# Optimization experiments

Measured on AMD Instinct MI355X. Metric: run time of the kernel, lower is better.

The kernel has to match this reference:

```python
import jax, jax.numpy as jnp
import numpy as np

HIDDEN = 2048
INTER = 4096
NUM_EXPERTS = 8
TOP_K = 4
BATCH, SEQ = 2, 2048
TOKENS = BATCH * SEQ


def setup_inputs() -> dict:
    key = jax.random.key(0)
    k_x, k_rw, k_tw, k_te, k_gu, k_dn = jax.random.split(key, 6)
    x = jax.random.normal(k_x, (BATCH, SEQ, HIDDEN), dtype=jnp.float32)
    # full router weights (passed through but unused by this patched forward)
    weights = jax.random.uniform(k_rw, (TOKENS, NUM_EXPERTS), dtype=jnp.float32)
    tw = jax.random.uniform(k_tw, (TOKENS, TOP_K), dtype=jnp.float32)
    top_weights = tw / jnp.sum(tw, axis=-1, keepdims=True)  # softmax-like, renormalize=False downstream
    top_experts = jax.random.randint(k_te, (TOKENS, TOP_K), 0, NUM_EXPERTS, dtype=jnp.int64)
    scale_gu = 1.0 / np.sqrt(HIDDEN)
    scale_dn = 1.0 / np.sqrt(INTER)
    gate_up_weights = jax.random.normal(k_gu, (NUM_EXPERTS, 2 * INTER, HIDDEN), dtype=jnp.float32) * scale_gu
    down_weights = jax.random.normal(k_dn, (NUM_EXPERTS, HIDDEN, INTER), dtype=jnp.float32) * scale_dn
    return {
        'x': x,
        'weights': weights,
        'top_weights': top_weights,
        'top_experts': top_experts,
        'gate_up_weights': gate_up_weights,
        'down_weights': down_weights,
    }


def _fused_moe(xf, gate_up_weights, down_weights, top_weights, top_experts):
    """xf: [T, D]. Dense per-expert loop (scan over experts), masked combine.

    Matches fused_moe(renormalize=False): out[t] = sum_k top_weights[t,k] * expert_{top_experts[t,k]}(x[t])
    expert(x) = (silu(x @ Wg^T) * (x @ Wu^T)) @ Wd^T with [Wg; Wu] = gate_up.
    """
    E = gate_up_weights.shape[0]

    def step(out, inp):
        w_gu, w_d, e = inp
        # per-token combine coefficient for this expert (0 if not routed)
        coef = jnp.sum(jnp.where(top_experts == e, top_weights, 0.0), axis=-1)  # [T]
        h = xf @ w_gu.T                       # [T, 2*INTER]
        gate, up = jnp.split(h, 2, axis=-1)
        act = jax.nn.silu(gate) * up          # [T, INTER]
        o = act @ w_d.T                       # [T, D]
        return out + coef[:, None] * o, None

    out, _ = jax.lax.scan(step, jnp.zeros_like(xf),
                          (gate_up_weights, down_weights, jnp.arange(E, dtype=jnp.int64)))
    return out


def reference(x, weights, top_weights, top_experts, gate_up_weights, down_weights):
    B, S, D = x.shape
    xf = x.reshape(-1, D)  # flatten(0, 1)
    out = _fused_moe(xf, gate_up_weights, down_weights, top_weights, top_experts)
    return out.reshape(B, S, D)  # unflatten(0, (-1, q_len))
```

## Files before the change

### kernel.cpp

```cpp
#include <hip/hip_runtime.h>
#include <stdint.h>

#define T_TOKENS 4096
#define D_HID    2048
#define D_INT    4096
#define N_EXP    8
#define TOPK     4
#define NFLAT    (T_TOKENS*TOPK)
#define BMT      256
#define MAXPAD   (NFLAT + N_EXP*BMT)
#define MT2      (MAXPAD/BMT)

#define OFF_PTOK 0ull
#define OFF_PWT  73728ull
#define OFF_CNT  147456ull
#define OFF_TOFF 147712ull
#define OFF_SEG  155904ull
#define OFF_XB   262144ull
#define OFF_ACT  17039360ull
#define OFF_W    168034304ull

typedef float f32x4  __attribute__((ext_vector_type(4)));
typedef short bf16x8 __attribute__((ext_vector_type(8)));

__device__ __forceinline__ unsigned short f2bf(float f) {
    unsigned int u = __float_as_uint(f);
    u += 0x7fffu + ((u >> 16) & 1u);
    return (unsigned short)(u >> 16);
}

__device__ __forceinline__ void gload_lds16(const void* g, void* l) {
    __builtin_amdgcn_global_load_lds((const __attribute__((address_space(1))) void*)g,
                                     (__attribute__((address_space(3))) void*)l,
                                     16, 0, 0);
}

__device__ __forceinline__ int xcd_logical(int hw, int nwg) {
    int q = nwg >> 3, r = nwg & 7;
    int xc = hw & 7, sl = hw >> 3;
    return (xc < r ? xc * (q + 1) : r * (q + 1) + (xc - r) * q) + sl;
}

__global__ void k_prep(const float* __restrict__ x, unsigned short* __restrict__ xb,
                       float* __restrict__ out) {
    const int N4 = T_TOKENS * D_HID / 4;
    for (int i = blockIdx.x * 256 + threadIdx.x; i < N4; i += 2048 * 256) {
        float4 v = ((const float4*)x)[i];
        ushort4 h;
        h.x = f2bf(v.x); h.y = f2bf(v.y); h.z = f2bf(v.z); h.w = f2bf(v.w);
        ((ushort4*)xb)[i] = h;
        ((float4*)out)[i] = make_float4(0.f, 0.f, 0.f, 0.f);
    }
}

__global__ void k_cast(const float* __restrict__ src, unsigned short* __restrict__ dst, int n4) {
    for (int i = blockIdx.x * 256 + threadIdx.x; i < n4; i += 2048 * 256) {
        float4 v = ((const float4*)src)[i];
        ushort4 h;
        h.x = f2bf(v.x); h.y = f2bf(v.y); h.z = f2bf(v.z); h.w = f2bf(v.w);
        ((ushort4*)dst)[i] = h;
    }
}

__global__ void k_count(const int* __restrict__ te, int* __restrict__ counts,
                        int* __restrict__ toff) {
    int e = blockIdx.x, t = threadIdx.x;
    int cnt = 0;
    int base = t * 64;
    for (int i = 0; i < 64; i++) cnt += (te[base + i] == e);
    __shared__ int s[256];
    s[t] = cnt; __syncthreads();
    int incl = cnt;
    for (int off = 1; off < 256; off <<= 1) {
        int tmp = (t >= off) ? s[t - off] : 0;
        __syncthreads();
        incl += tmp; s[t] = incl;
        __syncthreads();
    }
    toff[e * 256 + t] = incl - cnt;
    if (t == 255) counts[e] = incl;
}

__global__ void k_fill(const int* __restrict__ te, const float* __restrict__ tw,
                       const int* __restrict__ counts, const int* __restrict__ toff,
                       int* __restrict__ ptok, float* __restrict__ pwt, int* __restrict__ seg) {
    int e = blockIdx.x, t = threadIdx.x;
    int segs[9]; int a = 0;
    #pragma unroll
    for (int j = 0; j < 8; j++) { segs[j] = a; a += (counts[j] + BMT - 1) & ~(BMT - 1); }
    segs[8] = a;
    if (e == 0 && t == 0) { for (int j = 0; j < 9; j++) seg[j] = segs[j]; }
    int base = segs[e] + toff[e * 256 + t];
    int rank = 0;
    for (int i = t * 64; i < (t + 1) * 64; i++) {
        if (te[i] == e) { ptok[base + rank] = i >> 2; pwt[base + rank] = tw[i]; rank++; }
    }
    int cnt = counts[e], pc = (cnt + BMT - 1) & ~(BMT - 1);
    for (int i = cnt + t; i < pc; i += 256) { ptok[segs[e] + i] = -1; pwt[segs[e] + i] = 0.f; }
}


#define MFMA4(MI, AF) \
    _Pragma("unroll") for (int n_ = 0; n_ < 4; ++n_) \
        acc[MI][n_] = __builtin_amdgcn_mfma_f32_16x16x32_bf16(AF, bf[n_], acc[MI][n_], 0, 0, 0);

#define GATE8 asm volatile("s_waitcnt vmcnt(8)" ::: "memory");
#define GATE4 asm volatile("s_waitcnt vmcnt(4)" ::: "memory");
#define GATE0 asm volatile("s_waitcnt vmcnt(0)" ::: "memory");
#define GATEN

#define PH_A(DOSTAGE) \
  { \
    const char* pT = ldsc + (cb << 15); \
    _Pragma("unroll") for (int n_ = 0; n_ < 4; ++n_) \
        bf[n_] = *(const bf16x8*)(pT + b_off + n_ * 1024); \
    _Pragma("unroll") for (int m_ = 0; m_ < 4; ++m_) \
        af[m_] = *(const bf16x8*)(pT + a_off + m_ * 1024); \
    __builtin_amdgcn_sched_barrier(0); \
    if (DOSTAGE) { \
        char* d_ = ldsw + (sb << 15); \
        gload_lds16(pa0, d_ + dA0); gload_lds16(pa1, d_ + dA1); \
        pa0 += 64; pa1 += 64; \
    } \
    __builtin_amdgcn_sched_barrier(0); \
    __builtin_amdgcn_s_barrier(); \
    asm volatile("s_waitcnt lgkmcnt(0)" ::: "memory"); \
    __builtin_amdgcn_sched_barrier(0); \
    __builtin_amdgcn_s_setprio(1); \
    MFMA4(0, af[0]) MFMA4(1, af[1]) MFMA4(2, af[2]) MFMA4(3, af[3]) \
    __builtin_amdgcn_s_setprio(0); \
    __builtin_amdgcn_s_barrier(); \
  }

#define PH_B(DOSTAGE, GATE) \
  { \
    const char* pT = ldsc + (cb << 15); \
    _Pragma("unroll") for (int m_ = 0; m_ < 4; ++m_) \
        ag[m_] = *(const bf16x8*)(pT + a_off + 4096 + m_ * 1024); \
    __builtin_amdgcn_sched_barrier(0); \
    if (DOSTAGE) { \
        char* d_ = ldsw + (sb << 15); \
        gload_lds16(pb0, d_ + dB0); gload_lds16(pb1, d_ + dB1); \
        pb0 += 64; pb1 += 64; sb = (sb + 1) & 3; \
    } \
    GATE \
    __builtin_amdgcn_sched_barrier(0); \
    __builtin_amdgcn_s_barrier(); \
    asm volatile("s_waitcnt lgkmcnt(0)" ::: "memory"); \
    __builtin_amdgcn_sched_barrier(0); \
    __builtin_amdgcn_s_setprio(1); \
    MFMA4(4, ag[0]) MFMA4(5, ag[1]) MFMA4(6, ag[2]) MFMA4(7, ag[3]) \
    __builtin_amdgcn_s_setprio(0); \
    __builtin_amdgcn_s_barrier(); \
    cb = (cb + 1) & 3; \
  }

#define KLOOP \
    bf16x8 bf[4], af[4], ag[4]; \
    int cb = 0; \
    STAGE(); STAGE(); STAGE(); \
    asm volatile("s_waitcnt vmcnt(8)" ::: "memory"); \
    __builtin_amdgcn_s_barrier(); \
    for (int T = 0; T < 61; ++T) { PH_A(1) PH_B(1, GATE8) } \
    PH_A(0) PH_B(0, GATE4) \
    PH_A(0) PH_B(0, GATE0) \
    PH_A(0) PH_B(0, GATEN)

__global__ void __launch_bounds__(512, 2)
k_g1(const unsigned short* __restrict__ xb, const unsigned short* __restrict__ wgu_b,
     const int* __restrict__ ptok, const int* __restrict__ seg,
     unsigned short* __restrict__ act) {
    extern __shared__ char smem[];
    char* ldsw = smem; const char* ldsc = smem;
    int logical = xcd_logical(blockIdx.x, 2304);
    int nb = logical / MT2, mb = logical % MT2;
    if (mb * BMT >= seg[8]) return;
    int e = 0;
    #pragma unroll
    for (int j = 1; j < 8; ++j) if (seg[j] <= mb * BMT) e = j;
    int tid = threadIdx.x, w = tid >> 6, l = tid & 63;
    int wr = w >> 2, wc = w & 3;

    int g = (l & 3) ^ ((l >> 3) & 3);
    int r0 = w * 16 + (l >> 2), r1 = 128 + r0;
    int t0 = ptok[mb * BMT + r0]; if (t0 < 0) t0 = 0;
    int t1 = ptok[mb * BMT + r1]; if (t1 < 0) t1 = 0;
    const char* pa0 = (const char*)xb + (size_t)t0 * 4096 + g * 16;
    const char* pa1 = (const char*)xb + (size_t)t1 * 4096 + g * 16;
    int j0 = r0 & 63, j1 = r1 & 63;
    int gr0 = (j0 < 32) ? (nb * 128 + (r0 >> 6) * 32 + j0)
                        : (D_INT + nb * 128 + (r0 >> 6) * 32 + j0 - 32);
    int gr1 = (j1 < 32) ? (nb * 128 + (r1 >> 6) * 32 + j1)
                        : (D_INT + nb * 128 + (r1 >> 6) * 32 + j1 - 32);
    const char* wbase = (const char*)wgu_b + (size_t)e * 8192 * 4096;
    const char* pb0 = wbase + (size_t)gr0 * 4096 + g * 16;
    const char* pb1 = wbase + (size_t)gr1 * 4096 + g * 16;
    int dA0 = w * 1024, dA1 = 8192 + w * 1024;
    int dB0 = 16384 + w * 1024, dB1 = 24576 + w * 1024;
    int sb = 0;
    auto STAGE = [&]() {
        char* d = ldsw + (sb << 15);
        gload_lds16(pa0, d + dA0); gload_lds16(pa1, d + dA1);
        gload_lds16(pb0, d + dB0); gload_lds16(pb1, d + dB1);
        pa0 += 64; pa1 += 64; pb0 += 64; pb1 += 64;
        sb = (sb + 1) & 3;
    };

    int off_frag = (l & 15) * 64 + ((((l >> 4)) ^ (((l & 15) >> 1) & 3)) << 4);
    int a_off = wr * 8192 + off_frag;
    int b_off = 16384 + wc * 4096 + off_frag;

    f32x4 acc[8][4];
    #pragma unroll
    for (int m = 0; m < 8; ++m)
        #pragma unroll
        for (int n = 0; n < 4; ++n) acc[m][n] = (f32x4){0.f, 0.f, 0.f, 0.f};

    KLOOP

    int mbase = mb * BMT;
    #pragma unroll
    for (int m = 0; m < 8; ++m) {
        int rowl = wr * 128 + m * 16 + (l >> 4) * 4;
        #pragma unroll
        for (int np = 0; np < 2; ++np) {
            int col = nb * 128 + wc * 32 + np * 16 + (l & 15);
            #pragma unroll
            for (int r = 0; r < 4; ++r) {
                float gv = acc[m][np][r], uv = acc[m][np + 2][r];
                float av = gv / (1.f + __expf(-gv)) * uv;
                act[(size_t)(mbase + rowl + r) * D_INT + col] = f2bf(av);
            }
        }
    }
}

__global__ void __launch_bounds__(512, 2)
k_g2(const unsigned short* __restrict__ act, const unsigned short* __restrict__ wd_b,
     const int* __restrict__ ptok, const float* __restrict__ pwt,
     const int* __restrict__ seg, float* __restrict__ out) {
    extern __shared__ char smem[];
    char* ldsw = smem; const char* ldsc = smem;
    int logical = xcd_logical(blockIdx.x, 1152);
    int pair = logical / MT2, mb = logical % MT2;
    int nb = pair >> 1, ks = pair & 1;
    if (mb * BMT >= seg[8]) return;
    int e = 0;
    #pragma unroll
    for (int j = 1; j < 8; ++j) if (seg[j] <= mb * BMT) e = j;
    int tid = threadIdx.x, w = tid >> 6, l = tid & 63;
    int wr = w >> 2, wc = w & 3;
    int koff = ks * 4096;

    int g = (l & 3) ^ ((l >> 3) & 3);
    int r0 = w * 16 + (l >> 2), r1 = 128 + r0;
    const char* pa0 = (const char*)act + (size_t)(mb * BMT + r0) * 8192 + koff + g * 16;
    const char* pa1 = (const char*)act + (size_t)(mb * BMT + r1) * 8192 + koff + g * 16;
    const char* wbase = (const char*)wd_b + (size_t)e * D_HID * 8192;
    const char* pb0 = wbase + (size_t)(nb * 256 + r0) * 8192 + koff + g * 16;
    const char* pb1 = wbase + (size_t)(nb * 256 + r1) * 8192 + koff + g * 16;
    int dA0 = w * 1024, dA1 = 8192 + w * 1024;
    int dB0 = 16384 + w * 1024, dB1 = 24576 + w * 1024;
    int sb = 0;
    auto STAGE = [&]() {
        char* d = ldsw + (sb << 15);
        gload_lds16(pa0, d + dA0); gload_lds16(pa1, d + dA1);
        gload_lds16(pb0, d + dB0); gload_lds16(pb1, d + dB1);
        pa0 += 64; pa1 += 64; pb0 += 64; pb1 += 64;
        sb = (sb + 1) & 3;
    };

    int off_frag = (l & 15) * 64 + ((((l >> 4)) ^ (((l & 15) >> 1) & 3)) << 4);
    int a_off = wr * 8192 + off_frag;
    int b_off = 16384 + wc * 4096 + off_frag;

    f32x4 acc[8][4];
    #pragma unroll
    for (int m = 0; m < 8; ++m)
        #pragma unroll
        for (int n = 0; n < 4; ++n) acc[m][n] = (f32x4){0.f, 0.f, 0.f, 0.f};

    KLOOP

    #pragma unroll
    for (int m = 0; m < 8; ++m) {
        int rowl = wr * 128 + m * 16 + (l >> 4) * 4;
        #pragma unroll
        for (int r = 0; r < 4; ++r) {
            int p = mb * BMT + rowl + r;
            int tok = ptok[p];
            float wt = pwt[p];
            if (tok >= 0) {
                #pragma unroll
                for (int n = 0; n < 4; ++n) {
                    int col = nb * 256 + wc * 64 + n * 16 + (l & 15);
                    unsafeAtomicAdd(&out[(size_t)tok * D_HID + col], wt * acc[m][n][r]);
                }
            }
        }
    }
}

extern "C" void kernel_launch(void* const* d_in, const int* in_sizes, int n_in,
                              void* d_out, int out_size, void* d_ws, size_t ws_size,
                              hipStream_t stream) {
    const float* x   = (const float*)d_in[0];
    const float* tw  = (const float*)d_in[2];
    const int*   te  = (const int*)d_in[3];
    const float* wgu = (const float*)d_in[4];
    const float* wd  = (const float*)d_in[5];
    float* out = (float*)d_out;
    char*  ws  = (char*)d_ws;

    int*   ptok   = (int*)(ws + OFF_PTOK);
    float* pwt    = (float*)(ws + OFF_PWT);
    int*   counts = (int*)(ws + OFF_CNT);
    int*   toff   = (int*)(ws + OFF_TOFF);
    int*   seg    = (int*)(ws + OFF_SEG);
    unsigned short* xb  = (unsigned short*)(ws + OFF_XB);
    unsigned short* act = (unsigned short*)(ws + OFF_ACT);
    unsigned short* w_b = (unsigned short*)(ws + OFF_W);

    hipFuncSetAttribute((const void*)k_g1, hipFuncAttributeMaxDynamicSharedMemorySize, 131072);
    hipFuncSetAttribute((const void*)k_g2, hipFuncAttributeMaxDynamicSharedMemorySize, 131072);

    k_prep<<<2048, 256, 0, stream>>>(x, xb, out);
    k_count<<<N_EXP, 256, 0, stream>>>(te, counts, toff);
    k_fill<<<N_EXP, 256, 0, stream>>>(te, tw, counts, toff, ptok, pwt, seg);

    k_cast<<<2048, 256, 0, stream>>>(wgu, w_b, 33554432);
    k_g1<<<2304, 512, 131072, stream>>>(xb, w_b, ptok, seg, act);
    k_cast<<<2048, 256, 0, stream>>>(wd, w_b, 16777216);
    k_g2<<<1152, 512, 131072, stream>>>(act, w_b, ptok, pwt, seg, out);
}
```

Measured before the change: 1.277 ms.

## Switch GEMMs to 32x32x16 MFMA and deepen LDS pipeline to five stages

Both expert GEMM kernels move from 16x16x32 bf16 MFMA tiles to 32x32x16 tiles. This changes the LDS fragment offsets, the swizzle pattern and the epilogue row mapping. The K-loop also gets a fifth 32KB stage buffer (160KB of LDS), so one more global-to-LDS load stays in flight, with the wait thresholds adjusted to match. The larger MFMA shape is meant to cut LDS read traffic per FLOP and the number of issued instructions. The cost is higher LDS use, which with 160KB per block likely limits occupancy to one block per CU despite launch_bounds(512,2).

```diff
diff --git a/kernel.cpp b/kernel.cpp
--- a/kernel.cpp
+++ b/kernel.cpp
@@ -20,8 +20,9 @@
 #define OFF_ACT  17039360ull
 #define OFF_W    168034304ull
 
-typedef float f32x4  __attribute__((ext_vector_type(4)));
-typedef short bf16x8 __attribute__((ext_vector_type(8)));
+typedef float f32x4   __attribute__((ext_vector_type(4)));
+typedef float f32x16  __attribute__((ext_vector_type(16)));
+typedef short bf16x8  __attribute__((ext_vector_type(8)));
 
 __device__ __forceinline__ unsigned short f2bf(float f) {
     unsigned int u = __float_as_uint(f);
@@ -100,25 +101,27 @@
 }
 
 
-#define MFMA4(MI, AF) \
-    _Pragma("unroll") for (int n_ = 0; n_ < 4; ++n_) \
-        acc[MI][n_] = __builtin_amdgcn_mfma_f32_16x16x32_bf16(AF, bf[n_], acc[MI][n_], 0, 0, 0);
-
-#define GATE8 asm volatile("s_waitcnt vmcnt(8)" ::: "memory");
-#define GATE4 asm volatile("s_waitcnt vmcnt(4)" ::: "memory");
-#define GATE0 asm volatile("s_waitcnt vmcnt(0)" ::: "memory");
+#define MFMA8(AV, BV) \
+    _Pragma("unroll") for (int m_ = 0; m_ < 4; ++m_) \
+      _Pragma("unroll") for (int n_ = 0; n_ < 2; ++n_) \
+        acc[m_][n_] = __builtin_amdgcn_mfma_f32_32x32x16_bf16(AV[m_], BV[n_], acc[m_][n_], 0, 0, 0);
+
+#define GATE12 asm volatile("s_waitcnt vmcnt(12)" ::: "memory");
+#define GATE8  asm volatile("s_waitcnt vmcnt(8)" ::: "memory");
+#define GATE4  asm volatile("s_waitcnt vmcnt(4)" ::: "memory");
+#define GATE0  asm volatile("s_waitcnt vmcnt(0)" ::: "memory");
 #define GATEN
 
 #define PH_A(DOSTAGE) \
   { \
-    const char* pT = ldsc + (cb << 15); \
-    _Pragma("unroll") for (int n_ = 0; n_ < 4; ++n_) \
-        bf[n_] = *(const bf16x8*)(pT + b_off + n_ * 1024); \
+    const char* pT = ldsc + cb * 32768; \
+    _Pragma("unroll") for (int n_ = 0; n_ < 2; ++n_) \
+        bfr[n_] = *(const bf16x8*)(pT + boff + n_ * 2048 + ch0); \
     _Pragma("unroll") for (int m_ = 0; m_ < 4; ++m_) \
-        af[m_] = *(const bf16x8*)(pT + a_off + m_ * 1024); \
+        afr[m_] = *(const bf16x8*)(pT + aoff + m_ * 2048 + ch0); \
     __builtin_amdgcn_sched_barrier(0); \
     if (DOSTAGE) { \
-        char* d_ = ldsw + (sb << 15); \
+        char* d_ = ldsw + sb * 32768; \
         gload_lds16(pa0, d_ + dA0); gload_lds16(pa1, d_ + dA1); \
         pa0 += 64; pa1 += 64; \
     } \
@@ -127,21 +130,23 @@
     asm volatile("s_waitcnt lgkmcnt(0)" ::: "memory"); \
     __builtin_amdgcn_sched_barrier(0); \
     __builtin_amdgcn_s_setprio(1); \
-    MFMA4(0, af[0]) MFMA4(1, af[1]) MFMA4(2, af[2]) MFMA4(3, af[3]) \
+    MFMA8(afr, bfr) \
     __builtin_amdgcn_s_setprio(0); \
     __builtin_amdgcn_s_barrier(); \
   }
 
 #define PH_B(DOSTAGE, GATE) \
   { \
-    const char* pT = ldsc + (cb << 15); \
+    const char* pT = ldsc + cb * 32768; \
+    _Pragma("unroll") for (int n_ = 0; n_ < 2; ++n_) \
+        bgr[n_] = *(const bf16x8*)(pT + boff + n_ * 2048 + ch1); \
     _Pragma("unroll") for (int m_ = 0; m_ < 4; ++m_) \
-        ag[m_] = *(const bf16x8*)(pT + a_off + 4096 + m_ * 1024); \
+        agr[m_] = *(const bf16x8*)(pT + aoff + m_ * 2048 + ch1); \
     __builtin_amdgcn_sched_barrier(0); \
     if (DOSTAGE) { \
-        char* d_ = ldsw + (sb << 15); \
+        char* d_ = ldsw + sb * 32768; \
         gload_lds16(pb0, d_ + dB0); gload_lds16(pb1, d_ + dB1); \
-        pb0 += 64; pb1 += 64; sb = (sb + 1) & 3; \
+        pb0 += 64; pb1 += 64; sb = (sb == 4) ? 0 : sb + 1; \
     } \
     GATE \
     __builtin_amdgcn_sched_barrier(0); \
@@ -149,19 +154,20 @@
     asm volatile("s_waitcnt lgkmcnt(0)" ::: "memory"); \
     __builtin_amdgcn_sched_barrier(0); \
     __builtin_amdgcn_s_setprio(1); \
-    MFMA4(4, ag[0]) MFMA4(5, ag[1]) MFMA4(6, ag[2]) MFMA4(7, ag[3]) \
+    MFMA8(agr, bgr) \
     __builtin_amdgcn_s_setprio(0); \
     __builtin_amdgcn_s_barrier(); \
-    cb = (cb + 1) & 3; \
+    cb = (cb == 4) ? 0 : cb + 1; \
   }
 
 #define KLOOP \
-    bf16x8 bf[4], af[4], ag[4]; \
+    bf16x8 afr[4], bfr[2], agr[4], bgr[2]; \
     int cb = 0; \
-    STAGE(); STAGE(); STAGE(); \
-    asm volatile("s_waitcnt vmcnt(8)" ::: "memory"); \
-    __builtin_amdgcn_s_barrier(); \
-    for (int T = 0; T < 61; ++T) { PH_A(1) PH_B(1, GATE8) } \
+    STAGE(); STAGE(); STAGE(); STAGE(); \
+    asm volatile("s_waitcnt vmcnt(12)" ::: "memory"); \
+    __builtin_amdgcn_s_barrier(); \
+    for (int T = 0; T < 60; ++T) { PH_A(1) PH_B(1, GATE12) } \
+    PH_A(0) PH_B(0, GATE8) \
     PH_A(0) PH_B(0, GATE4) \
     PH_A(0) PH_B(0, GATE0) \
     PH_A(0) PH_B(0, GATEN)
@@ -181,7 +187,7 @@
     int tid = threadIdx.x, w = tid >> 6, l = tid & 63;
     int wr = w >> 2, wc = w & 3;
 
-    int g = (l & 3) ^ ((l >> 3) & 3);
+    int g = (l & 3) ^ ((l >> 2) & 3);
     int r0 = w * 16 + (l >> 2), r1 = 128 + r0;
     int t0 = ptok[mb * BMT + r0]; if (t0 < 0) t0 = 0;
     int t1 = ptok[mb * BMT + r1]; if (t1 < 0) t1 = 0;
@@ -199,38 +205,37 @@
     int dB0 = 16384 + w * 1024, dB1 = 24576 + w * 1024;
     int sb = 0;
     auto STAGE = [&]() {
-        char* d = ldsw + (sb << 15);
+        char* d = ldsw + sb * 32768;
         gload_lds16(pa0, d + dA0); gload_lds16(pa1, d + dA1);
         gload_lds16(pb0, d + dB0); gload_lds16(pb1, d + dB1);
         pa0 += 64; pa1 += 64; pb0 += 64; pb1 += 64;
-        sb = (sb + 1) & 3;
+        sb = (sb == 4) ? 0 : sb + 1;
     };
 
-    int off_frag = (l & 15) * 64 + ((((l >> 4)) ^ (((l & 15) >> 1) & 3)) << 4);
-    int a_off = wr * 8192 + off_frag;
-    int b_off = 16384 + wc * 4096 + off_frag;
-
-    f32x4 acc[8][4];
-    #pragma unroll
-    for (int m = 0; m < 8; ++m)
+    int hi = l >> 5;
+    int aoff = wr * 8192 + (l & 31) * 64;
+    int boff = 16384 + wc * 4096 + (l & 31) * 64;
+    int ch0 = ((hi) ^ (l & 3)) << 4;
+    int ch1 = ((2 | hi) ^ (l & 3)) << 4;
+
+    f32x16 acc[4][2];
+    #pragma unroll
+    for (int m = 0; m < 4; ++m)
         #pragma unroll
-        for (int n = 0; n < 4; ++n) acc[m][n] = (f32x4){0.f, 0.f, 0.f, 0.f};
+        for (int n = 0; n < 2; ++n) acc[m][n] = (f32x16)0.f;
 
     KLOOP
 
     int mbase = mb * BMT;
-    #pragma unroll
-    for (int m = 0; m < 8; ++m) {
-        int rowl = wr * 128 + m * 16 + (l >> 4) * 4;
+    int colg = nb * 128 + wc * 32 + (l & 31);
+    #pragma unroll
+    for (int m = 0; m < 4; ++m) {
         #pragma unroll
-        for (int np = 0; np < 2; ++np) {
-            int col = nb * 128 + wc * 32 + np * 16 + (l & 15);
-            #pragma unroll
-            for (int r = 0; r < 4; ++r) {
-                float gv = acc[m][np][r], uv = acc[m][np + 2][r];
-                float av = gv / (1.f + __expf(-gv)) * uv;
-                act[(size_t)(mbase + rowl + r) * D_INT + col] = f2bf(av);
-            }
+        for (int reg = 0; reg < 16; ++reg) {
+            int rowl = wr * 128 + m * 32 + (reg & 3) + 8 * (reg >> 2) + 4 * hi;
+            float gv = acc[m][0][reg], uv = acc[m][1][reg];
+            float av = gv / (1.f + __expf(-gv)) * uv;
+            act[(size_t)(mbase + rowl) * D_INT + colg] = f2bf(av);
         }
     }
 }
@@ -252,7 +257,7 @@
     int wr = w >> 2, wc = w & 3;
     int koff = ks * 4096;
 
-    int g = (l & 3) ^ ((l >> 3) & 3);
+    int g = (l & 3) ^ ((l >> 2) & 3);
     int r0 = w * 16 + (l >> 2), r1 = 128 + r0;
     const char* pa0 = (const char*)act + (size_t)(mb * BMT + r0) * 8192 + koff + g * 16;
     const char* pa1 = (const char*)act + (size_t)(mb * BMT + r1) * 8192 + koff + g * 16;
@@ -263,38 +268,39 @@
     int dB0 = 16384 + w * 1024, dB1 = 24576 + w * 1024;
     int sb = 0;
     auto STAGE = [&]() {
-        char* d = ldsw + (sb << 15);
+        char* d = ldsw + sb * 32768;
         gload_lds16(pa0, d + dA0); gload_lds16(pa1, d + dA1);
         gload_lds16(pb0, d + dB0); gload_lds16(pb1, d + dB1);
         pa0 += 64; pa1 += 64; pb0 += 64; pb1 += 64;
-        sb = (sb + 1) & 3;
+        sb = (sb == 4) ? 0 : sb + 1;
     };
 
-    int off_frag = (l & 15) * 64 + ((((l >> 4)) ^ (((l & 15) >> 1) & 3)) << 4);
-    int a_off = wr * 8192 + off_frag;
-    int b_off = 16384 + wc * 4096 + off_frag;
-
-    f32x4 acc[8][4];
-    #pragma unroll
-    for (int m = 0; m < 8; ++m)
+    int hi = l >> 5;
+    int aoff = wr * 8192 + (l & 31) * 64;
+    int boff = 16384 + wc * 4096 + (l & 31) * 64;
+    int ch0 = ((hi) ^ (l & 3)) << 4;
+    int ch1 = ((2 | hi) ^ (l & 3)) << 4;
+
+    f32x16 acc[4][2];
+    #pragma unroll
+    for (int m = 0; m < 4; ++m)
         #pragma unroll
-        for (int n = 0; n < 4; ++n) acc[m][n] = (f32x4){0.f, 0.f, 0.f, 0.f};
+        for (int n = 0; n < 2; ++n) acc[m][n] = (f32x16)0.f;
 
     KLOOP
 
     #pragma unroll
-    for (int m = 0; m < 8; ++m) {
-        int rowl = wr * 128 + m * 16 + (l >> 4) * 4;
+    for (int m = 0; m < 4; ++m) {
         #pragma unroll
-        for (int r = 0; r < 4; ++r) {
-            int p = mb * BMT + rowl + r;
+        for (int reg = 0; reg < 16; ++reg) {
+            int p = mb * BMT + wr * 128 + m * 32 + (reg & 3) + 8 * (reg >> 2) + 4 * hi;
             int tok = ptok[p];
             float wt = pwt[p];
             if (tok >= 0) {
                 #pragma unroll
-                for (int n = 0; n < 4; ++n) {
-                    int col = nb * 256 + wc * 64 + n * 16 + (l & 15);
-                    unsafeAtomicAdd(&out[(size_t)tok * D_HID + col], wt * acc[m][n][r]);
+                for (int nf = 0; nf < 2; ++nf) {
+                    int col = nb * 256 + wc * 64 + nf * 32 + (l & 31);
+                    unsafeAtomicAdd(&out[(size_t)tok * D_HID + col], wt * acc[m][nf][reg]);
                 }
             }
         }
@@ -321,15 +327,15 @@
     unsigned short* act = (unsigned short*)(ws + OFF_ACT);
     unsigned short* w_b = (unsigned short*)(ws + OFF_W);
 
-    hipFuncSetAttribute((const void*)k_g1, hipFuncAttributeMaxDynamicSharedMemorySize, 131072);
-    hipFuncSetAttribute((const void*)k_g2, hipFuncAttributeMaxDynamicSharedMemorySize, 131072);
+    hipFuncSetAttribute((const void*)k_g1, hipFuncAttributeMaxDynamicSharedMemorySize, 163840);
+    hipFuncSetAttribute((const void*)k_g2, hipFuncAttributeMaxDynamicSharedMemorySize, 163840);
 
     k_prep<<<2048, 256, 0, stream>>>(x, xb, out);
     k_count<<<N_EXP, 256, 0, stream>>>(te, counts, toff);
     k_fill<<<N_EXP, 256, 0, stream>>>(te, tw, counts, toff, ptok, pwt, seg);
 
     k_cast<<<2048, 256, 0, stream>>>(wgu, w_b, 33554432);
-    k_g1<<<2304, 512, 131072, stream>>>(xb, w_b, ptok, seg, act);
+    k_g1<<<2304, 512, 163840, stream>>>(xb, w_b, ptok, seg, act);
     k_cast<<<2048, 256, 0, stream>>>(wd, w_b, 16777216);
-    k_g2<<<1152, 512, 131072, stream>>>(act, w_b, ptok, pwt, seg, out);
-}
+    k_g2<<<1152, 512, 163840, stream>>>(act, w_b, ptok, pwt, seg, out);
+}
```

Result: slower. 1.526 ms (+19.5%).
